# Kernel tuning notes

Hardware: AMD Instinct MI355X
Metric: run time of the kernel (lower is better)

## Reference

```python
import jax, jax.numpy as jnp
import numpy as np

N = 30000      # nodes
IN = 768       # input feature dim
C = 128        # hidden channels (= conv out_dim, = gate dim)
HEADS = 4      # attention heads (TransformerConv and Semantic)
DH = 128       # per-head dim (concat=False -> out_channels)
R = 3          # num relations
E = 80000      # edges per relation
NEG = 0.01     # LeakyReLU slope


def setup_inputs() -> dict:
    key = jax.random.key(0)
    ks = iter(jax.random.split(key, 64))
    def nx(shape):
        return jax.random.normal(next(ks), shape, dtype=jnp.float32) * 0.02
    inp = {}
    inp["x"] = jax.random.normal(next(ks), (N, IN), dtype=jnp.float32)
    inp["edges"] = jax.random.randint(next(ks), (R, 2, E), 0, N, dtype=jnp.int32)
    inp["lin1_W"] = nx((IN, C)); inp["lin1_b"] = jnp.zeros((C,), jnp.float32)
    for l in ("l1", "l2"):
        inp[f"{l}_Wq"] = nx((R, C, HEADS * DH)); inp[f"{l}_bq"] = jnp.zeros((R, HEADS * DH), jnp.float32)
        inp[f"{l}_Wk"] = nx((R, C, HEADS * DH)); inp[f"{l}_bk"] = jnp.zeros((R, HEADS * DH), jnp.float32)
        inp[f"{l}_Wv"] = nx((R, C, HEADS * DH)); inp[f"{l}_bv"] = jnp.zeros((R, HEADS * DH), jnp.float32)
        inp[f"{l}_Ws"] = nx((R, C, DH));         inp[f"{l}_bs"] = jnp.zeros((R, DH), jnp.float32)
        inp[f"{l}_gW"] = nx((C + DH, C));        inp[f"{l}_gb"] = jnp.zeros((C,), jnp.float32)
        inp[f"{l}_sW1"] = nx((HEADS, C, C));     inp[f"{l}_sb1"] = jnp.zeros((HEADS, C), jnp.float32)
        inp[f"{l}_sw2"] = nx((HEADS, C))
    inp["lin2_W"] = nx((C, C)); inp["lin2_b"] = jnp.zeros((C,), jnp.float32)
    inp["clf_W"] = nx((C, 2)); inp["clf_b"] = jnp.zeros((2,), jnp.float32)
    return inp


def lrelu(x):
    return jnp.where(x >= 0, x, NEG * x)


def transformer_conv(x, src, dst, Wq, bq, Wk, bk, Wv, bv, Ws, bs):
    # PyG TransformerConv, heads=HEADS, concat=False (head mean), root_weight=True, eval (no dropout)
    n = x.shape[0]
    q = (x @ Wq + bq).reshape(n, HEADS, DH)
    k = (x @ Wk + bk).reshape(n, HEADS, DH)
    v = (x @ Wv + bv).reshape(n, HEADS, DH)
    logits = (q[dst] * k[src]).sum(-1) / np.sqrt(DH)      # [E, H]
    m = jax.ops.segment_max(logits, dst, num_segments=n)  # scatter-softmax (stable)
    a = jnp.exp(logits - m[dst])
    s = jax.ops.segment_sum(a, dst, num_segments=n)
    alpha = a / s[dst]
    agg = jax.ops.segment_sum(alpha[:, :, None] * v[src], dst, num_segments=n)  # [N, H, DH]
    return agg.mean(axis=1) + x @ Ws + bs


def semantic(Hm, sW1, sb1, sw2):
    # Hm: [N, R, C]; per-head scoring MLP -> softmax over relations -> weighted sum, averaged over heads
    t = jnp.tanh(jnp.einsum('nrc,hco->hnro', Hm, sW1) + sb1[:, None, None, :])  # [H, N, R, C]
    scores = jnp.einsum('hnro,ho->hnr', t, sw2).mean(axis=1)                    # [H, R]
    beta = jax.nn.softmax(scores, axis=-1)
    return jnp.einsum('hr,nrc->nc', beta, Hm) / HEADS


def rgt_layer(x, edges, Wq, bq, Wk, bk, Wv, bv, Ws, bs, gW, gb, sW1, sb1, sw2):
    Hs = []
    for r in range(R):  # small fixed relation loop
        src, dst = edges[r, 0], edges[r, 1]
        U = transformer_conv(x, src, dst, Wq[r], bq[r], Wk[r], bk[r], Wv[r], bv[r], Ws[r], bs[r])
        Z = jax.nn.sigmoid(jnp.concatenate([U, x], axis=1) @ gW + gb)
        Hs.append(jnp.tanh(U) * Z + x * (1.0 - Z))
    Hm = jnp.stack(Hs, axis=1)  # [N, R, C]
    return semantic(Hm, sW1, sb1, sw2)


def reference(x, edges, lin1_W, lin1_b,
              l1_Wq, l1_bq, l1_Wk, l1_bk, l1_Wv, l1_bv, l1_Ws, l1_bs, l1_gW, l1_gb, l1_sW1, l1_sb1, l1_sw2,
              l2_Wq, l2_bq, l2_Wk, l2_bk, l2_Wv, l2_bv, l2_Ws, l2_bs, l2_gW, l2_gb, l2_sW1, l2_sb1, l2_sw2,
              lin2_W, lin2_b, clf_W, clf_b):
    h = lrelu(x @ lin1_W + lin1_b)
    h = rgt_layer(h, edges, l1_Wq, l1_bq, l1_Wk, l1_bk, l1_Wv, l1_bv, l1_Ws, l1_bs, l1_gW, l1_gb, l1_sW1, l1_sb1, l1_sw2)
    h = rgt_layer(h, edges, l2_Wq, l2_bq, l2_Wk, l2_bk, l2_Wv, l2_bv, l2_Ws, l2_bs, l2_gW, l2_gb, l2_sW1, l2_sb1, l2_sw2)
    h = lrelu(h @ lin2_W + lin2_b)
    return h @ clf_W + clf_b
```

## Files before the change

kernel.cpp:

```cpp
#include <hip/hip_runtime.h>
#include <math.h>

#define Nn 30000
#define RR 3
#define EE 80000
#define MT_M 235

#define SAP 72
#define EP_LD 68
#define KBIG 0x40000000

typedef __attribute__((ext_vector_type(8))) short bf16x8;
typedef __attribute__((ext_vector_type(4))) float f32x4;

__device__ __forceinline__ unsigned short f2bf(float f) {
    union { float f; unsigned u; } v; v.f = f;
    unsigned r = v.u + 0x7fff + ((v.u >> 16) & 1);
    return (unsigned short)(r >> 16);
}
__device__ __forceinline__ float fast_tanh(float x) {
    float e = __expf(2.f * x);
    return 1.f - 2.f / (e + 1.f);
}
__device__ __forceinline__ void unpack8(uint4 u, float* f) {
    union { unsigned u; float f; } a;
    a.u = u.x << 16;          f[0] = a.f;
    a.u = u.x & 0xffff0000u;  f[1] = a.f;
    a.u = u.y << 16;          f[2] = a.f;
    a.u = u.y & 0xffff0000u;  f[3] = a.f;
    a.u = u.z << 16;          f[4] = a.f;
    a.u = u.z & 0xffff0000u;  f[5] = a.f;
    a.u = u.w << 16;          f[6] = a.f;
    a.u = u.w & 0xffff0000u;  f[7] = a.f;
}

__device__ __forceinline__ void mfma_core(
    const short* __restrict__ A, int lda,
    const short* __restrict__ A2, int lda2, int ksplit,
    const short* __restrict__ Bt,
    int M, int K, int m0, int n0,
    short* As, short* Bs, f32x4 (&acc)[4][4])
{
    const int t = threadIdx.x;
    const int srow = t >> 3;
    const int scol = (t & 7) << 3;
    const int lane = t & 63;
    const int wave = t >> 6;
    const int wm = (wave >> 1) << 6;
    const int wn = (wave & 1) << 6;
    const int fr = lane & 15;
    const int quad = lane >> 4;

    for (int k0 = 0; k0 < K; k0 += 64) {
        const short* Abase; int kk0, ldax;
        if (k0 < ksplit) { Abase = A;  kk0 = k0;          ldax = lda;  }
        else             { Abase = A2; kk0 = k0 - ksplit; ldax = lda2; }
        #pragma unroll
        for (int rr = 0; rr < 4; rr++) {
            int r = srow + rr * 32;
            int gr = m0 + r;
            bf16x8 va = {0, 0, 0, 0, 0, 0, 0, 0};
            if (gr < M) va = *(const bf16x8*)(Abase + (size_t)gr * ldax + kk0 + scol);
            *(bf16x8*)(As + r * SAP + scol) = va;
        }
        #pragma unroll
        for (int rr = 0; rr < 4; rr++) {
            int r = srow + rr * 32;
            bf16x8 vb = *(const bf16x8*)(Bt + (size_t)(n0 + r) * K + k0 + scol);
            *(bf16x8*)(Bs + r * SAP + scol) = vb;
        }
        __syncthreads();
        #pragma unroll
        for (int kc = 0; kc < 2; kc++) {
            bf16x8 af[4], bfr[4];
            #pragma unroll
            for (int i = 0; i < 4; i++)
                af[i] = *(const bf16x8*)(As + (wm + i * 16 + fr) * SAP + kc * 32 + quad * 8);
            #pragma unroll
            for (int i = 0; i < 4; i++)
                bfr[i] = *(const bf16x8*)(Bs + (wn + i * 16 + fr) * SAP + kc * 32 + quad * 8);
            #pragma unroll
            for (int mi = 0; mi < 4; mi++)
                #pragma unroll
                for (int ni = 0; ni < 4; ni++)
                    acc[mi][ni] = __builtin_amdgcn_mfma_f32_16x16x32_bf16(
                        af[mi], bfr[ni], acc[mi][ni], 0, 0, 0);
        }
        __syncthreads();
    }
}

__global__ __launch_bounds__(256) void gemm_mfma(
    const short* __restrict__ A, int lda,
    const short* __restrict__ A2, int lda2, int ksplit,
    const short* __restrict__ Bt, const float* __restrict__ bias,
    float* __restrict__ C, int ldc, short* __restrict__ Cbf, int ldcbf,
    int M, int K, int act)
{
    __shared__ short As[128 * SAP];
    __shared__ short Bs[128 * SAP];
    f32x4 acc[4][4];
    #pragma unroll
    for (int i = 0; i < 4; i++)
        #pragma unroll
        for (int j = 0; j < 4; j++) acc[i][j] = (f32x4){0.f, 0.f, 0.f, 0.f};
    int m0 = blockIdx.y * 128, n0 = blockIdx.x * 128;
    mfma_core(A, lda, A2, lda2, ksplit, Bt, M, K, m0, n0, As, Bs, acc);

    const int t = threadIdx.x;
    const int lane = t & 63, wave = t >> 6;
    const int wm = (wave >> 1) << 6, wn = (wave & 1) << 6;
    const int fr = lane & 15, quad = lane >> 4;
    float* ws = (float*)As + wave * 16 * EP_LD;
    const int rrow = lane >> 2;
    const int cseg = (lane & 3) << 4;
    #pragma unroll
    for (int mi = 0; mi < 4; mi++) {
        #pragma unroll
        for (int ni = 0; ni < 4; ni++)
            #pragma unroll
            for (int reg = 0; reg < 4; reg++)
                ws[(quad * 4 + reg) * EP_LD + ni * 16 + fr] = acc[mi][ni][reg];
        int gr = m0 + wm + mi * 16 + rrow;
        if (gr >= M) continue;
        int gc = n0 + wn + cseg;
        float vals[16];
        #pragma unroll
        for (int j = 0; j < 16; j++) {
            float v = ws[rrow * EP_LD + cseg + j] + bias[gc + j];
            if (act == 1) v = (v >= 0.f) ? v : 0.01f * v;
            vals[j] = v;
        }
        if (C) {
            float* cp = C + (size_t)gr * ldc + gc;
            #pragma unroll
            for (int j4 = 0; j4 < 4; j4++)
                *(float4*)(cp + j4 * 4) = make_float4(vals[j4 * 4], vals[j4 * 4 + 1],
                                                      vals[j4 * 4 + 2], vals[j4 * 4 + 3]);
        }
        if (Cbf) {
            unsigned pk[8];
            #pragma unroll
            for (int j2 = 0; j2 < 8; j2++)
                pk[j2] = ((unsigned)f2bf(vals[2 * j2 + 1]) << 16) | (unsigned)f2bf(vals[2 * j2]);
            unsigned* bp = (unsigned*)(Cbf + (size_t)gr * ldcbf + gc);
            *(uint4*)bp       = make_uint4(pk[0], pk[1], pk[2], pk[3]);
            *(uint4*)(bp + 4) = make_uint4(pk[4], pk[5], pk[6], pk[7]);
        }
    }
}

__global__ __launch_bounds__(256) void gemm_qkvs_v4(
    const short* __restrict__ A,
    const short* __restrict__ Wt, const float* __restrict__ bias,
    short* __restrict__ qhat3, short* __restrict__ Ubf, int M)
{
    __shared__ short As[128 * SAP];
    __shared__ short Bs[128 * SAP];
    f32x4 acc[4][4];
    #pragma unroll
    for (int i = 0; i < 4; i++)
        #pragma unroll
        for (int j = 0; j < 4; j++) acc[i][j] = (f32x4){0.f, 0.f, 0.f, 0.f};
    int m0 = blockIdx.y * 128, bx = blockIdx.x, n0 = bx * 128;
    mfma_core(A, 128, A, 128, KBIG, Wt, M, 128, m0, n0, As, Bs, acc);

    const int t = threadIdx.x;
    const int lane = t & 63, wave = t >> 6;
    const int wm = (wave >> 1) << 6, wn = (wave & 1) << 6;
    const int fr = lane & 15, quad = lane >> 4;
    float* ws = (float*)As + wave * 16 * EP_LD;
    const int rrow = lane >> 2;
    const int cseg = (lane & 3) << 4;
    #pragma unroll
    for (int mi = 0; mi < 4; mi++) {
        #pragma unroll
        for (int ni = 0; ni < 4; ni++)
            #pragma unroll
            for (int reg = 0; reg < 4; reg++)
                ws[(quad * 4 + reg) * EP_LD + ni * 16 + fr] = acc[mi][ni][reg];
        int gr = m0 + wm + mi * 16 + rrow;
        if (gr >= M) continue;
        int lc = wn + cseg;
        float vals[16];
        #pragma unroll
        for (int j = 0; j < 16; j++)
            vals[j] = ws[rrow * EP_LD + cseg + j] + bias[n0 + lc + j];
        unsigned pk[8];
        #pragma unroll
        for (int j2 = 0; j2 < 8; j2++)
            pk[j2] = ((unsigned)f2bf(vals[2 * j2 + 1]) << 16) | (unsigned)f2bf(vals[2 * j2]);
        short* dst;
        if (bx < 12) {
            int r = bx >> 2;
            dst = qhat3 + ((size_t)(r * Nn + gr)) * 512 + (bx - r * 4) * 128 + lc;
        } else {
            dst = Ubf + (size_t)gr * 384 + (bx - 12) * 128 + lc;
        }
        unsigned* bp = (unsigned*)dst;
        *(uint4*)bp       = make_uint4(pk[0], pk[1], pk[2], pk[3]);
        *(uint4*)(bp + 4) = make_uint4(pk[4], pk[5], pk[6], pk[7]);
    }
}

__global__ __launch_bounds__(256) void attn_v4(
    const short* __restrict__ qhat3, const short* __restrict__ hbf,
    const int* __restrict__ rowptr3, const int* __restrict__ col3,
    short* __restrict__ Ah3)
{
    int wid = ((blockIdx.x * blockDim.x + threadIdx.x) >> 6);
    int lane = threadIdx.x & 63;
    if (wid >= 3 * Nn) return;
    int r = wid / Nn, n = wid - r * Nn;
    const int* rowptr = rowptr3 + r * (Nn + 1);
    const int* colb = col3 + r * EE;
    int beg = rowptr[n], end = rowptr[n + 1];

    uint4 qv = ((const uint4*)(qhat3 + ((size_t)r * Nn + n) * 512))[lane];
    float qf[8];
    unpack8(qv, qf);
    const int l16 = lane & 15;

    float m = -INFINITY, s = 0.f;
    float acc[8] = {0.f, 0.f, 0.f, 0.f, 0.f, 0.f, 0.f, 0.f};

    for (int i = beg; i < end; i++) {
        int src = colb[i];
        uint4 hv = ((const uint4*)(hbf + (size_t)src * 128))[l16];
        float hf[8];
        unpack8(hv, hf);
        float p = qf[0] * hf[0] + qf[1] * hf[1] + qf[2] * hf[2] + qf[3] * hf[3]
                + qf[4] * hf[4] + qf[5] * hf[5] + qf[6] * hf[6] + qf[7] * hf[7];
        p += __shfl_xor(p, 1);
        p += __shfl_xor(p, 2);
        p += __shfl_xor(p, 4);
        p += __shfl_xor(p, 8);
        float nm = fmaxf(m, p);
        float sc = __expf(m - nm);
        float pe = __expf(p - nm);
        s = s * sc + pe;
        #pragma unroll
        for (int j = 0; j < 8; j++) acc[j] = acc[j] * sc + pe * hf[j];
        m = nm;
    }

    float inv = (s > 0.f) ? 1.f / s : 0.f;
    #pragma unroll
    for (int j = 0; j < 8; j++) acc[j] *= inv;

    unsigned p0 = ((unsigned)f2bf(acc[1]) << 16) | (unsigned)f2bf(acc[0]);
    unsigned p1 = ((unsigned)f2bf(acc[3]) << 16) | (unsigned)f2bf(acc[2]);
    unsigned p2 = ((unsigned)f2bf(acc[5]) << 16) | (unsigned)f2bf(acc[4]);
    unsigned p3 = ((unsigned)f2bf(acc[7]) << 16) | (unsigned)f2bf(acc[6]);
    *(uint4*)(Ah3 + ((size_t)r * Nn + n) * 512 + lane * 8) = make_uint4(p0, p1, p2, p3);
}

__global__ __launch_bounds__(256) void ufin_mfma(
    const short* __restrict__ Ah3, const short* __restrict__ wvst,
    const float* __restrict__ bvmean, const int* __restrict__ rowptr3,
    short* __restrict__ U_bf, int M)
{
    __shared__ short As[128 * SAP];
    __shared__ short Bs[128 * SAP];
    f32x4 acc[4][4];
    #pragma unroll
    for (int i = 0; i < 4; i++)
        #pragma unroll
        for (int j = 0; j < 4; j++) acc[i][j] = (f32x4){0.f, 0.f, 0.f, 0.f};
    int r = blockIdx.z;
    int m0 = blockIdx.y * 128;
    const short* Ar = Ah3 + (size_t)r * Nn * 512;
    mfma_core(Ar, 512, Ar, 512, KBIG, wvst + r * 65536, M, 512, m0, 0, As, Bs, acc);

    const int t = threadIdx.x;
    const int lane = t & 63, wave = t >> 6;
    const int wm = (wave >> 1) << 6, wn = (wave & 1) << 6;
    const int fr = lane & 15, quad = lane >> 4;
    float* ws = (float*)As + wave * 16 * EP_LD;
    const int rrow = lane >> 2;
    const int cseg = (lane & 3) << 4;
    #pragma unroll
    for (int mi = 0; mi < 4; mi++) {
        #pragma unroll
        for (int ni = 0; ni < 4; ni++)
            #pragma unroll
            for (int reg = 0; reg < 4; reg++)
                ws[(quad * 4 + reg) * EP_LD + ni * 16 + fr] = acc[mi][ni][reg];
        int gr = m0 + wm + mi * 16 + rrow;
        if (gr >= M) continue;
        int gc = wn + cseg;
        int be = rowptr3[r * (Nn + 1) + gr];
        int en = rowptr3[r * (Nn + 1) + gr + 1];
        float mk = (en > be) ? 1.f : 0.f;
        short* up = U_bf + (size_t)gr * 384 + r * 128 + gc;
        uint4 u0 = *(const uint4*)up;
        uint4 u1 = *(const uint4*)(up + 8);
        float uv[16];
        unpack8(u0, uv); unpack8(u1, uv + 8);
        float vals[16];
        #pragma unroll
        for (int j = 0; j < 16; j++)
            vals[j] = ws[rrow * EP_LD + cseg + j] + uv[j] + mk * bvmean[r * 128 + gc + j];
        unsigned pk[8];
        #pragma unroll
        for (int j2 = 0; j2 < 8; j2++)
            pk[j2] = ((unsigned)f2bf(vals[2 * j2 + 1]) << 16) | (unsigned)f2bf(vals[2 * j2]);
        unsigned* bp = (unsigned*)up;
        *(uint4*)bp       = make_uint4(pk[0], pk[1], pk[2], pk[3]);
        *(uint4*)(bp + 4) = make_uint4(pk[4], pk[5], pk[6], pk[7]);
    }
}

__global__ __launch_bounds__(256) void gate_mfma(
    const short* __restrict__ Ubf,
    const short* __restrict__ Hbf,
    const short* __restrict__ gWt, const float* __restrict__ gb,
    const float* __restrict__ Hf,
    float* __restrict__ Hm, short* __restrict__ HmBf,
    int M)
{
    __shared__ short As[128 * SAP];
    __shared__ short Bs[128 * SAP];
    f32x4 acc[4][4];
    #pragma unroll
    for (int i = 0; i < 4; i++)
        #pragma unroll
        for (int j = 0; j < 4; j++) acc[i][j] = (f32x4){0.f, 0.f, 0.f, 0.f};
    int r = blockIdx.z;
    int m0 = blockIdx.y * 128;
    mfma_core(Ubf + r * 128, 384, Hbf, 128, 128, gWt, M, 256, m0, 0, As, Bs, acc);

    const int t = threadIdx.x;
    const int lane = t & 63, wave = t >> 6;
    const int wm = (wave >> 1) << 6, wn = (wave & 1) << 6;
    const int fr = lane & 15, quad = lane >> 4;
    float* ws = (float*)As + wave * 16 * EP_LD;
    const int rrow = lane >> 2;
    const int cseg = (lane & 3) << 4;
    #pragma unroll
    for (int mi = 0; mi < 4; mi++) {
        #pragma unroll
        for (int ni = 0; ni < 4; ni++)
            #pragma unroll
            for (int reg = 0; reg < 4; reg++)
                ws[(quad * 4 + reg) * EP_LD + ni * 16 + fr] = acc[mi][ni][reg];
        int gr = m0 + wm + mi * 16 + rrow;
        if (gr >= M) continue;
        int gc = wn + cseg;
        const short* up = Ubf + (size_t)gr * 384 + r * 128 + gc;
        const float* hp = Hf + (size_t)gr * 128 + gc;
        float uv[16], hv[16];
        uint4 u0 = *(const uint4*)up;
        uint4 u1 = *(const uint4*)(up + 8);
        unpack8(u0, uv); unpack8(u1, uv + 8);
        #pragma unroll
        for (int j4 = 0; j4 < 4; j4++)
            *(float4*)(hv + j4 * 4) = *(const float4*)(hp + j4 * 4);
        float vals[16];
        #pragma unroll
        for (int j = 0; j < 16; j++) {
            float g = ws[rrow * EP_LD + cseg + j] + gb[gc + j];
            float z = 1.f / (1.f + __expf(-g));
            vals[j] = fast_tanh(uv[j]) * z + hv[j] * (1.f - z);
        }
        float* cp = Hm + (size_t)gr * 384 + r * 128 + gc;
        #pragma unroll
        for (int j4 = 0; j4 < 4; j4++)
            *(float4*)(cp + j4 * 4) = make_float4(vals[j4 * 4], vals[j4 * 4 + 1],
                                                  vals[j4 * 4 + 2], vals[j4 * 4 + 3]);
        unsigned pk[8];
        #pragma unroll
        for (int j2 = 0; j2 < 8; j2++)
            pk[j2] = ((unsigned)f2bf(vals[2 * j2 + 1]) << 16) | (unsigned)f2bf(vals[2 * j2]);
        unsigned* bp = (unsigned*)(HmBf + (size_t)gr * 384 + r * 128 + gc);
        *(uint4*)bp       = make_uint4(pk[0], pk[1], pk[2], pk[3]);
        *(uint4*)(bp + 4) = make_uint4(pk[4], pk[5], pk[6], pk[7]);
    }
}

__global__ __launch_bounds__(256) void semantic_mfma(
    const short* __restrict__ HmBf, const short* __restrict__ sW1t,
    const float* __restrict__ sb1, const float* __restrict__ sw2,
    float* __restrict__ partial, int M)
{
    __shared__ short As[128 * SAP];
    __shared__ short Bs[128 * SAP];
    __shared__ float red4[4];
    f32x4 acc[4][4];
    #pragma unroll
    for (int i = 0; i < 4; i++)
        #pragma unroll
        for (int j = 0; j < 4; j++) acc[i][j] = (f32x4){0.f, 0.f, 0.f, 0.f};
    int head = blockIdx.x, r = blockIdx.z;
    int m0 = blockIdx.y * 128, n0 = head * 128;
    mfma_core(HmBf + r * 128, 384, HmBf + r * 128, 384, KBIG, sW1t, M, 128, m0, n0, As, Bs, acc);
    const int t = threadIdx.x;
    const int lane = t & 63, wave = t >> 6;
    const int wm = (wave >> 1) << 6, wn = (wave & 1) << 6;
    const int fr = lane & 15, quad = lane >> 4;
    float local = 0.f;
    #pragma unroll
    for (int ni = 0; ni < 4; ni++) {
        int gc = n0 + wn + ni * 16 + fr;
        float b = sb1[gc], w2 = sw2[gc];
        #pragma unroll
        for (int mi = 0; mi < 4; mi++) {
            #pragma unroll
            for (int reg = 0; reg < 4; reg++) {
                int gr = m0 + wm + mi * 16 + quad * 4 + reg;
                if (gr >= M) continue;
                local += fast_tanh(acc[mi][ni][reg] + b) * w2;
            }
        }
    }
    #pragma unroll
    for (int off = 1; off < 64; off <<= 1) local += __shfl_xor(local, off);
    if (lane == 0) red4[wave] = local;
    __syncthreads();
    if (t == 0)
        partial[(head * 3 + r) * MT_M + blockIdx.y] = red4[0] + red4[1] + red4[2] + red4[3];
}

__global__ void reduce12_kernel(const float* __restrict__ partial, float* __restrict__ scores)
{
    int z = blockIdx.x;
    int lane = threadIdx.x;
    float s = 0.f;
    for (int i = lane; i < MT_M; i += 64) s += partial[z * MT_M + i];
    #pragma unroll
    for (int off = 1; off < 64; off <<= 1) s += __shfl_xor(s, off);
    if (lane == 0) scores[z] = s;
}

__global__ void compute_w_kernel(const float* __restrict__ scores, float* __restrict__ w, float invN)
{
    if (blockIdx.x == 0 && threadIdx.x == 0) {
        float wr[3] = {0.f, 0.f, 0.f};
        for (int h = 0; h < 4; h++) {
            float s0 = scores[h * 3 + 0] * invN;
            float s1 = scores[h * 3 + 1] * invN;
            float s2 = scores[h * 3 + 2] * invN;
            float mx = fmaxf(s0, fmaxf(s1, s2));
            float e0 = __expf(s0 - mx), e1 = __expf(s1 - mx), e2 = __expf(s2 - mx);
            float inv = 1.f / (e0 + e1 + e2);
            wr[0] += 0.25f * e0 * inv;
            wr[1] += 0.25f * e1 * inv;
            wr[2] += 0.25f * e2 * inv;
        }
        w[0] = wr[0]; w[1] = wr[1]; w[2] = wr[2];
    }
}

__global__ void mix_kernel(const float* __restrict__ Hm, const float* __restrict__ w,
                           float* __restrict__ h, short* __restrict__ hbf, int total4)
{
    int i = blockIdx.x * blockDim.x + threadIdx.x;
    if (i >= total4) return;
    int n = i >> 5, c4 = (i & 31) << 2;
    const float* row = Hm + (size_t)n * 384 + c4;
    float4 a = *(const float4*)row;
    float4 b = *(const float4*)(row + 128);
    float4 c = *(const float4*)(row + 256);
    float w0 = w[0], w1 = w[1], w2 = w[2];
    float4 v = make_float4(w0 * a.x + w1 * b.x + w2 * c.x,
                           w0 * a.y + w1 * b.y + w2 * c.y,
                           w0 * a.z + w1 * b.z + w2 * c.z,
                           w0 * a.w + w1 * b.w + w2 * c.w);
    *(float4*)(h + (size_t)n * 128 + c4) = v;
    unsigned p0 = ((unsigned)f2bf(v.y) << 16) | (unsigned)f2bf(v.x);
    unsigned p1 = ((unsigned)f2bf(v.w) << 16) | (unsigned)f2bf(v.z);
    *(uint2*)(hbf + (size_t)n * 128 + c4) = make_uint2(p0, p1);
}

__global__ void convert_bf16_kernel(const float* __restrict__ src, unsigned* __restrict__ dst, int n_pairs)
{
    int i = blockIdx.x * blockDim.x + threadIdx.x;
    if (i >= n_pairs) return;
    float2 f = ((const float2*)src)[i];
    dst[i] = ((unsigned)f2bf(f.y) << 16) | (unsigned)f2bf(f.x);
}

__global__ void prep_global_kernel(const float* __restrict__ lin1_W, const float* __restrict__ lin2_W,
                                   short* __restrict__ lin1Wt, short* __restrict__ lin2Wt)
{
    int id = blockIdx.x * blockDim.x + threadIdx.x;
    if (id < 98304) {
        int n = id / 768, k = id % 768;
        lin1Wt[id] = (short)f2bf(lin1_W[k * 128 + n]);
    } else if (id < 114688) {
        int r = id - 98304;
        int n = r / 128, k = r % 128;
        lin2Wt[r] = (short)f2bf(lin2_W[k * 128 + n]);
    }
}

__global__ void prep_layer_v4(
    const float* __restrict__ Ws, const float* __restrict__ bs,
    const float* __restrict__ gW, const float* __restrict__ sW1,
    const float* __restrict__ Wv, const float* __restrict__ bv,
    short* __restrict__ Wt4, short* __restrict__ gWt,
    short* __restrict__ sW1t, short* __restrict__ wvst,
    float* __restrict__ B4, float* __restrict__ bvmean)
{
    const int S0 = 49152;
    const int S1 = S0 + 32768;
    const int S2 = S1 + 65536;
    const int S3 = S2 + 196608;
    const int S4 = S3 + 384;
    const int S5 = S4 + 384;
    int id = blockIdx.x * blockDim.x + threadIdx.x;
    if (id < S0) {
        int n = id / 128, k = id - n * 128;
        int r = n >> 7, c = n & 127;
        Wt4[(size_t)(1536 + n) * 128 + k] = (short)f2bf(Ws[(size_t)r * 16384 + k * 128 + c]);
    } else if (id < S1) {
        int q = id - S0;
        int n = q / 256, k = q - n * 256;
        gWt[q] = (short)f2bf(gW[k * 128 + n]);
    } else if (id < S2) {
        int q = id - S1;
        int h = q / 16384, rem = q - h * 16384;
        int n = rem / 128, k = rem - n * 128;
        sW1t[q] = (short)f2bf(sW1[(size_t)h * 16384 + k * 128 + n]);
    } else if (id < S3) {
        int q = id - S2;
        int r = q / 65536, rem = q - r * 65536;
        int d = rem / 512, mcol = rem - d * 512;
        int hh = mcol >> 7, j = mcol & 127;
        wvst[q] = (short)f2bf(0.25f * Wv[(size_t)r * 65536 + j * 512 + hh * 128 + d]);
    } else if (id < S4) {
        int q = id - S3;
        B4[1536 + q] = bs[q];
    } else if (id < S5) {
        int q = id - S4;
        int r = q >> 7, d = q & 127;
        bvmean[q] = 0.25f * (bv[r * 512 + d] + bv[r * 512 + 128 + d]
                           + bv[r * 512 + 256 + d] + bv[r * 512 + 384 + d]);
    }
}

__global__ __launch_bounds__(256) void gmat_kernel(
    const float* __restrict__ Wq0, const float* __restrict__ Wk0, const float* __restrict__ bq0,
    const float* __restrict__ Wq1, const float* __restrict__ Wk1, const float* __restrict__ bq1,
    short* __restrict__ Wt4, float* __restrict__ B4)
{
    __shared__ float WqL[128 * 128];
    __shared__ float WkL[128 * 128];
    int h = blockIdx.x, r = blockIdx.y, l = blockIdx.z;
    const float* Wq = l ? Wq1 : Wq0;
    const float* Wk = l ? Wk1 : Wk0;
    const float* bq = l ? bq1 : bq0;
    short* Wt = Wt4 + (size_t)l * 245760;
    float* Bb = B4 + l * 1920;
    const float scale = 0.088388347648318447f;
    int t = threadIdx.x;
    for (int idx = t; idx < 16384; idx += 256) {
        int a = idx >> 7, b = idx & 127;
        WqL[idx] = Wq[(size_t)r * 65536 + b * 512 + h * 128 + a];
        WkL[idx] = Wk[(size_t)r * 65536 + a * 512 + h * 128 + b];
    }
    __syncthreads();
    for (int out = t; out < 16384; out += 256) {
        int i = out & 127, j = out >> 7;
        float dot = 0.f;
        #pragma unroll 8
        for (int d = 0; d < 128; d++)
            dot += WqL[d * 128 + i] * WkL[j * 128 + d];
        Wt[(size_t)(r * 512 + h * 128 + j) * 128 + i] = (short)f2bf(scale * dot);
    }
    if (t < 128) {
        const float* bqh = bq + r * 512 + h * 128;
        float c = 0.f;
        for (int d = 0; d < 128; d++) c += bqh[d] * WkL[t * 128 + d];
        Bb[r * 512 + h * 128 + t] = scale * c;
    }
}

__global__ void zero_i32_kernel(int* __restrict__ p, int n)
{
    int i = blockIdx.x * blockDim.x + threadIdx.x;
    if (i < n) p[i] = 0;
}

__global__ void hist3_kernel(const int* __restrict__ edges, int* __restrict__ cnt3)
{
    int i = blockIdx.x * blockDim.x + threadIdx.x;
    if (i >= 3 * EE) return;
    int r = i / EE, e = i - r * EE;
    int d = edges[(size_t)r * 2 * EE + EE + e];
    atomicAdd(&cnt3[r * Nn + d], 1);
}

__global__ __launch_bounds__(1024) void scan3_kernel(const int* __restrict__ cnt3,
                                                     int* __restrict__ rowptr3)
{
    __shared__ int part[1024];
    const int r = blockIdx.x;
    const int* cnt = cnt3 + r * Nn;
    int* rowptr = rowptr3 + r * (Nn + 1);
    int tid = threadIdx.x;
    int per = (Nn + 1023) >> 10;
    int base = tid * per;
    int s = 0;
    for (int i = 0; i < per; i++) {
        int idx = base + i;
        if (idx < Nn) s += cnt[idx];
    }
    part[tid] = s;
    __syncthreads();
    for (int off = 1; off < 1024; off <<= 1) {
        int val = (tid >= off) ? part[tid - off] : 0;
        __syncthreads();
        part[tid] += val;
        __syncthreads();
    }
    int excl = (tid == 0) ? 0 : part[tid - 1];
    for (int i = 0; i < per; i++) {
        int idx = base + i;
        if (idx < Nn) { rowptr[idx] = excl; excl += cnt[idx]; }
    }
    if (tid == 1023) rowptr[Nn] = part[1023];
}

__global__ void scatter3_kernel(const int* __restrict__ edges,
                                const int* __restrict__ rowptr3, int* __restrict__ fill3,
                                int* __restrict__ col3)
{
    int i = blockIdx.x * blockDim.x + threadIdx.x;
    if (i >= 3 * EE) return;
    int r = i / EE, e = i - r * EE;
    int src = edges[(size_t)r * 2 * EE + e];
    int d   = edges[(size_t)r * 2 * EE + EE + e];
    int pos = rowptr3[r * (Nn + 1) + d] + atomicAdd(&fill3[r * Nn + d], 1);
    col3[r * EE + pos] = src;
}

__global__ void clf_kernel(const float* __restrict__ t, const float* __restrict__ W,
                           const float* __restrict__ b, float* __restrict__ out, int M)
{
    int n = blockIdx.x * blockDim.x + threadIdx.x;
    if (n >= M) return;
    const float* row = t + (size_t)n * 128;
    float a0 = b[0], a1 = b[1];
    #pragma unroll
    for (int kk = 0; kk < 128; kk++) {
        float a = row[kk];
        a0 += a * W[kk * 2];
        a1 += a * W[kk * 2 + 1];
    }
    out[n * 2] = a0;
    out[n * 2 + 1] = a1;
}

extern "C" void kernel_launch(void* const* d_in, const int* in_sizes, int n_in,
                              void* d_out, int out_size, void* d_ws, size_t ws_size,
                              hipStream_t stream)
{
    const float* x      = (const float*)d_in[0];
    const int*   edges  = (const int*)d_in[1];
    const float* lin1_W = (const float*)d_in[2];
    const float* lin1_b = (const float*)d_in[3];
    const int L0 = 4, L1 = 17;
    const float* lin2_W = (const float*)d_in[30];
    const float* lin2_b = (const float*)d_in[31];
    const float* clf_W  = (const float*)d_in[32];
    const float* clf_b  = (const float*)d_in[33];
    float* out = (float*)d_out;

    char* w = (char*)d_ws;
    size_t off = 0;
    auto alloc = [&](size_t bytes) { void* p = w + off; off = (off + bytes + 255) & ~(size_t)255; return p; };
    float* h      = (float*)alloc((size_t)Nn * 128 * 4);
    short* h_bf   = (short*)alloc((size_t)Nn * 128 * 2);
    short* U_bf   = (short*)alloc((size_t)Nn * 384 * 2);
    const size_t QH = (size_t)3 * Nn * 512 * 2;
    char* BIG     = (char*)alloc(2 * QH);
    short* qhat3  = (short*)BIG;
    short* Ah3    = (short*)(BIG + QH);
    short* x_bf   = (short*)BIG;
    float* Hm     = (float*)BIG;
    short* Hm_bf  = (short*)(BIG + (size_t)Nn * 384 * 4);
    float* lin2o  = (float*)BIG;
    short* lin1Wt = (short*)alloc((size_t)98304 * 2);
    short* lin2Wt = (short*)alloc((size_t)16384 * 2);
    short* qkvsWt4 = (short*)alloc((size_t)2 * 245760 * 2);
    short* gWt    = (short*)alloc((size_t)2 * 32768 * 2);
    short* sW1t   = (short*)alloc((size_t)2 * 65536 * 2);
    short* wvst   = (short*)alloc((size_t)2 * 196608 * 2);
    float* qkvsB4 = (float*)alloc((size_t)2 * 1920 * 4);
    float* bvmean = (float*)alloc((size_t)2 * 384 * 4);
    int* rowptr3  = (int*)alloc((size_t)3 * (Nn + 1) * 4);
    int* cnt3     = (int*)alloc((size_t)3 * Nn * 4);
    int* col3     = (int*)alloc((size_t)3 * EE * 4);
    float* partial = (float*)alloc((size_t)12 * MT_M * 4);
    float* scores = (float*)alloc(12 * 4);
    float* wmix   = (float*)alloc(3 * 4);

    const int MT = MT_M;
    dim3 blk(256);

    {
        int n_pairs = Nn * 768 / 2;
        convert_bf16_kernel<<<(n_pairs + 255) / 256, blk, 0, stream>>>(x, (unsigned*)x_bf, n_pairs);
        prep_global_kernel<<<(114688 + 255) / 256, blk, 0, stream>>>(lin1_W, lin2_W, lin1Wt, lin2Wt);
        for (int l = 0; l < 2; l++) {
            int base = (l == 0) ? L0 : L1;
            prep_layer_v4<<<(344832 + 255) / 256, blk, 0, stream>>>(
                (const float*)d_in[base + 6], (const float*)d_in[base + 7],
                (const float*)d_in[base + 8], (const float*)d_in[base + 10],
                (const float*)d_in[base + 4], (const float*)d_in[base + 5],
                qkvsWt4 + (size_t)l * 245760, gWt + (size_t)l * 32768,
                sW1t + (size_t)l * 65536, wvst + (size_t)l * 196608,
                qkvsB4 + (size_t)l * 1920, bvmean + (size_t)l * 384);
        }
        gmat_kernel<<<dim3(4, 3, 2), blk, 0, stream>>>(
            (const float*)d_in[L0 + 0], (const float*)d_in[L0 + 2], (const float*)d_in[L0 + 1],
            (const float*)d_in[L1 + 0], (const float*)d_in[L1 + 2], (const float*)d_in[L1 + 1],
            qkvsWt4, qkvsB4);
        zero_i32_kernel<<<(3 * Nn + 255) / 256, blk, 0, stream>>>(cnt3, 3 * Nn);
        hist3_kernel<<<(3 * EE + 255) / 256, blk, 0, stream>>>(edges, cnt3);
        scan3_kernel<<<3, 1024, 0, stream>>>(cnt3, rowptr3);
        zero_i32_kernel<<<(3 * Nn + 255) / 256, blk, 0, stream>>>(cnt3, 3 * Nn);
        scatter3_kernel<<<(3 * EE + 255) / 256, blk, 0, stream>>>(edges, rowptr3, cnt3, col3);
    }

    gemm_mfma<<<dim3(1, MT), blk, 0, stream>>>(
        x_bf, 768, x_bf, 768, KBIG, lin1Wt, lin1_b, h, 128, h_bf, 128, Nn, 768, 1);

    for (int l = 0; l < 2; l++) {
        int base = (l == 0) ? L0 : L1;
        const float* gb  = (const float*)d_in[base + 9];
        const float* sb1 = (const float*)d_in[base + 11];
        const float* sw2 = (const float*)d_in[base + 12];
        short* lWt4   = qkvsWt4 + (size_t)l * 245760;
        short* lgWt   = gWt + (size_t)l * 32768;
        short* lsW1t  = sW1t + (size_t)l * 65536;
        short* lwvst  = wvst + (size_t)l * 196608;
        float* lB4    = qkvsB4 + (size_t)l * 1920;
        float* lbvm   = bvmean + (size_t)l * 384;

        gemm_qkvs_v4<<<dim3(15, MT), blk, 0, stream>>>(
            h_bf, lWt4, lB4, qhat3, U_bf, Nn);

        attn_v4<<<(3 * Nn + 3) / 4, blk, 0, stream>>>(qhat3, h_bf, rowptr3, col3, Ah3);

        ufin_mfma<<<dim3(1, MT, 3), blk, 0, stream>>>(Ah3, lwvst, lbvm, rowptr3, U_bf, Nn);

        gate_mfma<<<dim3(1, MT, 3), blk, 0, stream>>>(
            U_bf, h_bf, lgWt, gb, h, Hm, Hm_bf, Nn);

        semantic_mfma<<<dim3(4, MT, 3), blk, 0, stream>>>(Hm_bf, lsW1t, sb1, sw2, partial, Nn);
        reduce12_kernel<<<12, 64, 0, stream>>>(partial, scores);
        compute_w_kernel<<<1, 64, 0, stream>>>(scores, wmix, 1.f / (float)Nn);
        mix_kernel<<<(Nn * 32 + 255) / 256, blk, 0, stream>>>(Hm, wmix, h, h_bf, Nn * 32);
    }

    gemm_mfma<<<dim3(1, MT), blk, 0, stream>>>(
        h_bf, 128, h_bf, 128, KBIG, lin2Wt, lin2_b, lin2o, 128, (short*)nullptr, 0, Nn, 128, 1);
    clf_kernel<<<(Nn + 255) / 256, blk, 0, stream>>>(lin2o, clf_W, clf_b, out, Nn);
}
```

Measured before the change: 907.5 us.

## Split gmat Wq·Wk^T precompute across more blocks with register tiling

The per-head Wq·Wk^T fold kernel previously ran on only 24 blocks, each computing a full 128x128 product with strided scalar global loads. It now launches 192 blocks, each handling 16 output columns. Loads are coalesced float4 reads into a padded shared tile to avoid bank conflicts, and each thread accumulates 8 outputs in registers. The aim is to cut latency of this small weight-prep kernel by using far more of the GPU, at the cost of reloading the Wq tile in each of the 8 column-group blocks.

```diff
diff --git a/kernel.cpp b/kernel.cpp
--- a/kernel.cpp
+++ b/kernel.cpp
@@ -539,40 +539,60 @@
     }
 }
 
-__global__ __launch_bounds__(256) void gmat_kernel(
+__global__ __launch_bounds__(256) void gmat_v2(
     const float* __restrict__ Wq0, const float* __restrict__ Wk0, const float* __restrict__ bq0,
     const float* __restrict__ Wq1, const float* __restrict__ Wk1, const float* __restrict__ bq1,
     short* __restrict__ Wt4, float* __restrict__ B4)
 {
-    __shared__ float WqL[128 * 128];
-    __shared__ float WkL[128 * 128];
-    int h = blockIdx.x, r = blockIdx.y, l = blockIdx.z;
+    __shared__ float WqL[128 * 129];
+    __shared__ float WkL[16 * 128];
+    const int jg = blockIdx.x;
+    const int h  = blockIdx.y;
+    const int lz = blockIdx.z;
+    const int l = lz / 3, r = lz - l * 3;
     const float* Wq = l ? Wq1 : Wq0;
     const float* Wk = l ? Wk1 : Wk0;
     const float* bq = l ? bq1 : bq0;
     short* Wt = Wt4 + (size_t)l * 245760;
     float* Bb = B4 + l * 1920;
     const float scale = 0.088388347648318447f;
-    int t = threadIdx.x;
-    for (int idx = t; idx < 16384; idx += 256) {
-        int a = idx >> 7, b = idx & 127;
-        WqL[idx] = Wq[(size_t)r * 65536 + b * 512 + h * 128 + a];
-        WkL[idx] = Wk[(size_t)r * 65536 + a * 512 + h * 128 + b];
+    const int t = threadIdx.x;
+
+    for (int v = t; v < 4096; v += 256) {
+        int i = v >> 5, d4 = (v & 31) << 2;
+        float4 q = *(const float4*)(Wq + (size_t)r * 65536 + i * 512 + h * 128 + d4);
+        float* wp = WqL + i * 129 + d4;
+        wp[0] = q.x; wp[1] = q.y; wp[2] = q.z; wp[3] = q.w;
+    }
+    for (int v = t; v < 512; v += 256) {
+        int jl = v >> 5, d4 = (v & 31) << 2;
+        float4 q = *(const float4*)(Wk + (size_t)r * 65536 + (jg * 16 + jl) * 512 + h * 128 + d4);
+        float* wp = WkL + jl * 128 + d4;
+        wp[0] = q.x; wp[1] = q.y; wp[2] = q.z; wp[3] = q.w;
     }
     __syncthreads();
-    for (int out = t; out < 16384; out += 256) {
-        int i = out & 127, j = out >> 7;
-        float dot = 0.f;
-        #pragma unroll 8
-        for (int d = 0; d < 128; d++)
-            dot += WqL[d * 128 + i] * WkL[j * 128 + d];
-        Wt[(size_t)(r * 512 + h * 128 + j) * 128 + i] = (short)f2bf(scale * dot);
-    }
-    if (t < 128) {
+
+    const int i = t & 127;
+    const int jh = t >> 7;
+    const float* wk = WkL + jh * 8 * 128;
+    float acc[8] = {0.f, 0.f, 0.f, 0.f, 0.f, 0.f, 0.f, 0.f};
+    #pragma unroll 4
+    for (int d = 0; d < 128; d++) {
+        float wq = WqL[i * 129 + d];
+        #pragma unroll
+        for (int jj = 0; jj < 8; jj++)
+            acc[jj] += wq * wk[jj * 128 + d];
+    }
+    short* wrow = Wt + ((size_t)(r * 512 + h * 128 + jg * 16 + jh * 8)) * 128 + i;
+    #pragma unroll
+    for (int jj = 0; jj < 8; jj++)
+        wrow[(size_t)jj * 128] = (short)f2bf(scale * acc[jj]);
+
+    if (t < 16) {
         const float* bqh = bq + r * 512 + h * 128;
         float c = 0.f;
         for (int d = 0; d < 128; d++) c += bqh[d] * WkL[t * 128 + d];
-        Bb[r * 512 + h * 128 + t] = scale * c;
+        Bb[r * 512 + h * 128 + jg * 16 + t] = scale * c;
     }
 }
 
@@ -713,7 +733,7 @@
                 sW1t + (size_t)l * 65536, wvst + (size_t)l * 196608,
                 qkvsB4 + (size_t)l * 1920, bvmean + (size_t)l * 384);
         }
-        gmat_kernel<<<dim3(4, 3, 2), blk, 0, stream>>>(
+        gmat_v2<<<dim3(8, 4, 6), blk, 0, stream>>>(
             (const float*)d_in[L0 + 0], (const float*)d_in[L0 + 2], (const float*)d_in[L0 + 1],
             (const float*)d_in[L1 + 0], (const float*)d_in[L1 + 2], (const float*)d_in[L1 + 1],
             qkvsWt4, qkvsB4);
```

After: 812.5 us. 10.5% less time.
